# Performance work log

Hardware: AMD Instinct MI355X
Metric: run time of the kernel (lower is better)

The kernel has to match this reference:

```python
import jax, jax.numpy as jnp
import numpy as np

B, T, FIN, D = 8, 512, 256, 128


def setup_inputs() -> dict:
    key = jax.random.key(0)
    ks = jax.random.split(key, 12)
    s = lambda fan_in: 1.0 / np.sqrt(fan_in)
    return {
        "x": jax.random.normal(ks[0], (B, T, FIN), jnp.float32),
        "S0": jnp.zeros((B, 1, D, D), jnp.float32),
        "Z0": jnp.zeros((B, 1, D), jnp.float32),
        "gamma": jnp.ones((FIN,), jnp.float32),
        "beta": jnp.zeros((FIN,), jnp.float32),
        "Wk": jax.random.normal(ks[1], (FIN, D), jnp.float32) * s(FIN),
        "Wq": jax.random.normal(ks[2], (FIN, D), jnp.float32) * s(FIN),
        "Wv": jax.random.normal(ks[3], (FIN, D), jnp.float32) * s(FIN),
        "W1": jax.random.normal(ks[4], (D, D), jnp.float32) * s(D),
        "b1": jnp.zeros((D,), jnp.float32),
        "W2": jax.random.normal(ks[5], (D, D), jnp.float32) * s(D),
        "b2": jnp.zeros((D,), jnp.float32),
        "Ws": jax.random.normal(ks[6], (FIN, D), jnp.float32) * s(FIN),
        "bs": jnp.zeros((D,), jnp.float32),
    }


def reference(x, S0, Z0, gamma, beta, Wk, Wq, Wv, W1, b1, W2, b2, Ws, bs):
    CLAMP = 1e20
    # LayerNorm over feature dim
    mu = jnp.mean(x, axis=-1, keepdims=True)
    var = jnp.var(x, axis=-1, keepdims=True)
    xn = (x - mu) / jnp.sqrt(var + 1e-5) * gamma + beta
    # phi(x) = elu(x) + 1
    K = jax.nn.elu(xn @ Wk) + 1.0  # [B,T,D]
    Q = jax.nn.elu(xn @ Wq) + 1.0  # [B,T,D]
    V = xn @ Wv                     # [B,T,D]
    # outer-product state recurrence via cumsum (faithful to original)
    outer = jnp.einsum('bti,btj->btij', K, V)            # [B,T,D,D]
    S = jnp.clip(jnp.cumsum(outer, axis=1), -CLAMP, CLAMP) + S0  # [B,T,D,D]
    Z = jnp.clip(jnp.cumsum(K, axis=1), -CLAMP, CLAMP) + Z0      # [B,T,D]
    numerator = jnp.einsum('bti,btil->btl', Q, S)        # [B,T,D]
    denominator = jnp.einsum('bti,bti->bt', Q, Z)[..., None] + 1e-5
    out = numerator / denominator
    # FFN: relu(relu(out W1 + b1) W2 + b2)
    out = jax.nn.relu(jax.nn.relu(out @ W1 + b1) @ W2 + b2)
    # residual shortcut from normed input
    out = out + xn @ Ws + bs
    S_out = S.reshape(B, T, D * D)
    return out, S_out, Z
```

## Files before the change

kernel.cpp:

```cpp
#include <hip/hip_runtime.h>


constexpr int BB = 8, TT = 512, FIN_ = 256, DD = 128;
constexpr int NROW = BB * TT;
constexpr int CLEN = 64, NCH = 8;
constexpr float CLAMPV = 1e20f;

__global__ __launch_bounds__(256) void ln_kernel(
    const float* __restrict__ x, const float* __restrict__ gamma,
    const float* __restrict__ beta, float* __restrict__ xn)
{
  int row = blockIdx.x, tid = threadIdx.x;
  float v = x[row * FIN_ + tid];
  __shared__ float s1[256], s2[256];
  s1[tid] = v; s2[tid] = v * v;
  __syncthreads();
  for (int s = 128; s > 0; s >>= 1) {
    if (tid < s) { s1[tid] += s1[tid + s]; s2[tid] += s2[tid + s]; }
    __syncthreads();
  }
  float mu  = s1[0] * (1.0f / FIN_);
  float var = s2[0] * (1.0f / FIN_) - mu * mu;
  float rs  = rsqrtf(var + 1e-5f);
  xn[row * FIN_ + tid] = (v - mu) * rs * gamma[tid] + beta[tid];
}

__global__ __launch_bounds__(256) void gemm_qkvs(
    const float* __restrict__ xn,
    const float* __restrict__ Wk, const float* __restrict__ Wq,
    const float* __restrict__ Wv, const float* __restrict__ Ws,
    const float* __restrict__ bs,
    float* __restrict__ Kb, float* __restrict__ Qb,
    float* __restrict__ Vb, float* __restrict__ Rb)
{
  int ct = blockIdx.x, rt = blockIdx.y;
  int mat = ct >> 1, cb = (ct & 1) * 64;
  const float* W = (mat == 0) ? Wk : (mat == 1) ? Wq : (mat == 2) ? Wv : Ws;
  float* Ob      = (mat == 0) ? Kb : (mat == 1) ? Qb : (mat == 2) ? Vb : Rb;
  __shared__ float As[16][64];
  __shared__ float Bs[16][64];
  int tid = threadIdx.x;
  int tn = tid & 15, tm = tid >> 4;
  int lm = tid >> 2, lq = tid & 3;
  int lk = tid >> 4, ln4 = (tid & 15) * 4;
  float acc[4][4] = {};
  for (int k0 = 0; k0 < FIN_; k0 += 16) {
    float4 av = *(const float4*)&xn[(rt * 64 + lm) * FIN_ + k0 + lq * 4];
    As[lq * 4 + 0][lm] = av.x;
    As[lq * 4 + 1][lm] = av.y;
    As[lq * 4 + 2][lm] = av.z;
    As[lq * 4 + 3][lm] = av.w;
    *(float4*)&Bs[lk][ln4] = *(const float4*)&W[(k0 + lk) * DD + cb + ln4];
    __syncthreads();
#pragma unroll
    for (int k = 0; k < 16; k++) {
      float4 a = *(const float4*)&As[k][tm * 4];
      float4 b = *(const float4*)&Bs[k][tn * 4];
      float ar[4] = {a.x, a.y, a.z, a.w};
      float br[4] = {b.x, b.y, b.z, b.w};
#pragma unroll
      for (int i = 0; i < 4; i++)
#pragma unroll
        for (int j = 0; j < 4; j++) acc[i][j] += ar[i] * br[j];
    }
    __syncthreads();
  }
#pragma unroll
  for (int i = 0; i < 4; i++) {
    int row = rt * 64 + tm * 4 + i;
    int col = cb + tn * 4;
    float vals[4];
#pragma unroll
    for (int j = 0; j < 4; j++) {
      float v = acc[i][j];
      if (mat <= 1) v = (v > 0.f) ? v + 1.f : expf(v);
      else if (mat == 3) v += bs[col + j];
      vals[j] = v;
    }
    float4 o = make_float4(vals[0], vals[1], vals[2], vals[3]);
    *(float4*)&Ob[row * DD + col] = o;
  }
}

__global__ __launch_bounds__(256) void chunksum_kernel(
    const float* __restrict__ Kb, const float* __restrict__ Vb,
    float* __restrict__ chunkS, float* __restrict__ chunkz)
{
  int c = blockIdx.x, b = blockIdx.y, tid = threadIdx.x;
  __shared__ float Ks[CLEN][DD];
  const float* Kc = Kb + (b * TT + c * CLEN) * DD;
  const float* Vc = Vb + (b * TT + c * CLEN) * DD;
  for (int u = 0; u < 8; u++) {
    int idx = u * 256 + tid;
    int t = idx >> 5, c4 = (idx & 31) * 4;
    *(float4*)&Ks[t][c4] = *(const float4*)&Kc[t * DD + c4];
  }
  __syncthreads();
  int ti = tid >> 4, tj = tid & 15;
  int i0 = ti * 8, j0 = tj * 8;
  float acc[8][8] = {};
  for (int t = 0; t < CLEN; t++) {
    float kv[8], vv[8];
    *(float4*)&kv[0] = *(const float4*)&Ks[t][i0];
    *(float4*)&kv[4] = *(const float4*)&Ks[t][i0 + 4];
    *(float4*)&vv[0] = *(const float4*)&Vc[t * DD + j0];
    *(float4*)&vv[4] = *(const float4*)&Vc[t * DD + j0 + 4];
#pragma unroll
    for (int i = 0; i < 8; i++)
#pragma unroll
      for (int j = 0; j < 8; j++) acc[i][j] += kv[i] * vv[j];
  }
  float* oS = chunkS + (b * NCH + c) * DD * DD;
#pragma unroll
  for (int i = 0; i < 8; i++) {
    *(float4*)&oS[(i0 + i) * DD + j0]     = *(float4*)&acc[i][0];
    *(float4*)&oS[(i0 + i) * DD + j0 + 4] = *(float4*)&acc[i][4];
  }
  if (tid < DD) {
    float z = 0.f;
    for (int t = 0; t < CLEN; t++) z += Ks[t][tid];
    chunkz[(b * NCH + c) * DD + tid] = z;
  }
}

__global__ __launch_bounds__(256) void scan_s_kernel(
    const float* __restrict__ chunkS, const float* __restrict__ S0,
    float* __restrict__ prefS)
{
  int b = blockIdx.y;
  int idx = blockIdx.x * 256 + threadIdx.x;
  float s0v = S0[b * DD * DD + idx];
  float acc = 0.f;
  for (int c = 0; c < NCH; c++) {
    prefS[(b * NCH + c) * DD * DD + idx] = acc + s0v;
    acc += chunkS[(b * NCH + c) * DD * DD + idx];
  }
}

__global__ __launch_bounds__(128) void scan_z_kernel(
    const float* __restrict__ chunkz, const float* __restrict__ Z0,
    float* __restrict__ prefz)
{
  int b = blockIdx.x, i = threadIdx.x;
  float z0v = Z0[b * DD + i];
  float acc = 0.f;
  for (int c = 0; c < NCH; c++) {
    prefz[(b * NCH + c) * DD + i] = acc + z0v;
    acc += chunkz[(b * NCH + c) * DD + i];
  }
}

__global__ __launch_bounds__(256) void s_write_kernel(
    const float* __restrict__ Kb, const float* __restrict__ Vb,
    const float* __restrict__ prefS, float* __restrict__ Sout)
{
  int jt = blockIdx.x, c = blockIdx.y, b = blockIdx.z;
  __shared__ float Ks[CLEN][DD];
  __shared__ float Vs[CLEN][32];
  int tid = threadIdx.x;
  const float* Kc = Kb + (b * TT + c * CLEN) * DD;
  const float* Vc = Vb + (b * TT + c * CLEN) * DD + jt * 32;
  for (int u = 0; u < 8; u++) {
    int idx = u * 256 + tid;
    int t = idx >> 5, c4 = (idx & 31) * 4;
    *(float4*)&Ks[t][c4] = *(const float4*)&Kc[t * DD + c4];
  }
  for (int u = 0; u < 2; u++) {
    int idx = u * 256 + tid;
    int t = idx >> 3, c4 = (idx & 7) * 4;
    *(float4*)&Vs[t][c4] = *(const float4*)&Vc[t * DD + c4];
  }
  __syncthreads();
  int jq = tid & 7, irow = tid >> 3;
  int j = jt * 32 + jq * 4;
  float4 pref[4], acc[4];
#pragma unroll
  for (int p = 0; p < 4; p++) {
    int i = irow + 32 * p;
    pref[p] = *(const float4*)&prefS[(b * NCH + c) * DD * DD + i * DD + j];
    acc[p] = make_float4(0.f, 0.f, 0.f, 0.f);
  }
  float* So = Sout + (size_t)(b * TT + c * CLEN) * (DD * DD);
  for (int t = 0; t < CLEN; t++) {
    float4 v4 = *(const float4*)&Vs[t][jq * 4];
#pragma unroll
    for (int p = 0; p < 4; p++) {
      int i = irow + 32 * p;
      float kk = Ks[t][i];
      acc[p].x += kk * v4.x; acc[p].y += kk * v4.y;
      acc[p].z += kk * v4.z; acc[p].w += kk * v4.w;
      float4 o;
      o.x = fminf(fmaxf(pref[p].x + acc[p].x, -CLAMPV), CLAMPV);
      o.y = fminf(fmaxf(pref[p].y + acc[p].y, -CLAMPV), CLAMPV);
      o.z = fminf(fmaxf(pref[p].z + acc[p].z, -CLAMPV), CLAMPV);
      o.w = fminf(fmaxf(pref[p].w + acc[p].w, -CLAMPV), CLAMPV);
      *(float4*)&So[(size_t)t * (DD * DD) + i * DD + j] = o;
    }
  }
}

__global__ __launch_bounds__(256) void attn_a_kernel(
    const float* __restrict__ Kb, const float* __restrict__ Qb,
    const float* __restrict__ prefz, float* __restrict__ scores,
    float* __restrict__ Zout)
{
  int c = blockIdx.x, b = blockIdx.y, tid = threadIdx.x;
  __shared__ float KsT[DD][CLEN + 1];
  __shared__ float sc[CLEN][65];
  __shared__ float zeff[DD];
  const float* Kc = Kb + (b * TT + c * CLEN) * DD;
  const float* Qc = Qb + (b * TT + c * CLEN) * DD;
  for (int u = 0; u < 8; u++) {
    int idx = u * 256 + tid;
    int t = idx >> 5, c4 = (idx & 31) * 4;
    float4 v = *(const float4*)&Kc[t * DD + c4];
    KsT[c4 + 0][t] = v.x; KsT[c4 + 1][t] = v.y;
    KsT[c4 + 2][t] = v.z; KsT[c4 + 3][t] = v.w;
  }
  if (tid < DD) zeff[tid] = prefz[(b * NCH + c) * DD + tid];
  __syncthreads();
  int tn = tid & 15, tm = tid >> 4;
  float s[4][4] = {};
  for (int k4 = 0; k4 < 32; k4++) {
    float qv[4][4];
#pragma unroll
    for (int i = 0; i < 4; i++)
      *(float4*)&qv[i][0] = *(const float4*)&Qc[(tm * 4 + i) * DD + k4 * 4];
#pragma unroll
    for (int kk = 0; kk < 4; kk++) {
      int k = k4 * 4 + kk;
      float kv[4];
#pragma unroll
      for (int j = 0; j < 4; j++) kv[j] = KsT[k][tn * 4 + j];
#pragma unroll
      for (int i = 0; i < 4; i++)
#pragma unroll
        for (int j = 0; j < 4; j++) s[i][j] += qv[i][kk] * kv[j];
    }
  }
#pragma unroll
  for (int i = 0; i < 4; i++)
#pragma unroll
    for (int j = 0; j < 4; j++) {
      int t = tm * 4 + i, tau = tn * 4 + j;
      sc[t][tau] = (tau <= t) ? s[i][j] : 0.f;
    }
  __syncthreads();
  float* scg = scores + (b * NCH + c) * (CLEN * CLEN);
  for (int u = 0; u < 16; u++) {
    int idx = u * 256 + tid;
    scg[idx] = sc[idx >> 6][idx & 63];
  }
  if (tid < DD) {
    int i = tid;
    float a = zeff[i];
    for (int t = 0; t < CLEN; t++) {
      a += KsT[i][t];
      Zout[(size_t)(b * TT + c * CLEN + t) * DD + i] = fminf(fmaxf(a, -CLAMPV), CLAMPV);
    }
  }
}

__global__ __launch_bounds__(256) void attn_b_kernel(
    const float* __restrict__ Qb, const float* __restrict__ Vb,
    const float* __restrict__ prefS, const float* __restrict__ prefz,
    const float* __restrict__ scores, float* __restrict__ attn_o)
{
  int c = blockIdx.x, b = blockIdx.y, tid = threadIdx.x;
  __shared__ float Qs[CLEN][129];
  __shared__ float sc[CLEN][65];
  __shared__ float zeff[DD];
  __shared__ float den[CLEN];
  const float* Qc = Qb + (b * TT + c * CLEN) * DD;
  const float* Vc = Vb + (b * TT + c * CLEN) * DD;
  for (int u = 0; u < 8; u++) {
    int idx = u * 256 + tid;
    int t = idx >> 5, c4 = (idx & 31) * 4;
    float4 v = *(const float4*)&Qc[t * DD + c4];
    Qs[t][c4 + 0] = v.x; Qs[t][c4 + 1] = v.y;
    Qs[t][c4 + 2] = v.z; Qs[t][c4 + 3] = v.w;
  }
  const float* scg = scores + (b * NCH + c) * CLEN * CLEN;
  for (int u = 0; u < 16; u++) {
    int idx = u * 256 + tid;
    sc[idx >> 6][idx & 63] = scg[idx];
  }
  if (tid < DD) zeff[tid] = prefz[(b * NCH + c) * DD + tid];
  __syncthreads();
  if (tid < CLEN) {
    int t = tid;
    float d = 0.f;
    for (int tau = 0; tau < CLEN; tau++) d += sc[t][tau];
    float dz = 0.f;
    for (int k = 0; k < DD; k++) dz += Qs[t][k] * zeff[k];
    den[t] = d + dz + 1e-5f;
  }
  __syncthreads();
  int tl = tid & 31, tt = tid >> 5;
  int l0 = tl * 4, t0 = tt * 8;
  float num[8][4] = {};
  for (int tau = 0; tau < CLEN; tau++) {
    float4 v4 = *(const float4*)&Vc[tau * DD + l0];
    float ss[8];
#pragma unroll
    for (int ii = 0; ii < 8; ii++) ss[ii] = sc[t0 + ii][tau];
#pragma unroll
    for (int ii = 0; ii < 8; ii++) {
      num[ii][0] += ss[ii] * v4.x; num[ii][1] += ss[ii] * v4.y;
      num[ii][2] += ss[ii] * v4.z; num[ii][3] += ss[ii] * v4.w;
    }
  }
  const float* P = prefS + (b * NCH + c) * DD * DD;
  for (int i = 0; i < DD; i++) {
    float4 p4 = *(const float4*)&P[i * DD + l0];
    float qq[8];
#pragma unroll
    for (int ii = 0; ii < 8; ii++) qq[ii] = Qs[t0 + ii][i];
#pragma unroll
    for (int ii = 0; ii < 8; ii++) {
      num[ii][0] += qq[ii] * p4.x; num[ii][1] += qq[ii] * p4.y;
      num[ii][2] += qq[ii] * p4.z; num[ii][3] += qq[ii] * p4.w;
    }
  }
  float* og = attn_o + (size_t)(b * TT + c * CLEN) * DD;
#pragma unroll
  for (int ii = 0; ii < 8; ii++) {
    float dd = den[t0 + ii];
    float4 o = make_float4(num[ii][0] / dd, num[ii][1] / dd,
                           num[ii][2] / dd, num[ii][3] / dd);
    *(float4*)&og[(t0 + ii) * DD + l0] = o;
  }
}

__global__ __launch_bounds__(256) void ffn_kernel(
    const float* __restrict__ att, const float* __restrict__ res,
    const float* __restrict__ W1, const float* __restrict__ b1,
    const float* __restrict__ W2, const float* __restrict__ b2,
    float* __restrict__ outp)
{
  int rt = blockIdx.x, tid = threadIdx.x;
  __shared__ float As[32][129];
  __shared__ float H1[32][129];
  const float* ab = att + rt * 32 * DD;
  for (int u = 0; u < 4; u++) {
    int idx = u * 256 + tid;
    int r = idx >> 5, c4 = (idx & 31) * 4;
    float4 v = *(const float4*)&ab[r * DD + c4];
    As[r][c4 + 0] = v.x; As[r][c4 + 1] = v.y;
    As[r][c4 + 2] = v.z; As[r][c4 + 3] = v.w;
  }
  __syncthreads();
  int cn = tid & 31, rm = tid >> 5;
  int col = cn * 4, r0 = rm * 4;
  float acc[4][4] = {};
  for (int k = 0; k < DD; k++) {
    float4 w = *(const float4*)&W1[k * DD + col];
    float a[4];
#pragma unroll
    for (int i = 0; i < 4; i++) a[i] = As[r0 + i][k];
#pragma unroll
    for (int i = 0; i < 4; i++) {
      acc[i][0] += a[i] * w.x; acc[i][1] += a[i] * w.y;
      acc[i][2] += a[i] * w.z; acc[i][3] += a[i] * w.w;
    }
  }
  float4 bv = *(const float4*)&b1[col];
#pragma unroll
  for (int i = 0; i < 4; i++) {
    H1[r0 + i][col + 0] = fmaxf(acc[i][0] + bv.x, 0.f);
    H1[r0 + i][col + 1] = fmaxf(acc[i][1] + bv.y, 0.f);
    H1[r0 + i][col + 2] = fmaxf(acc[i][2] + bv.z, 0.f);
    H1[r0 + i][col + 3] = fmaxf(acc[i][3] + bv.w, 0.f);
  }
  __syncthreads();
  float acc2[4][4] = {};
  for (int k = 0; k < DD; k++) {
    float4 w = *(const float4*)&W2[k * DD + col];
    float a[4];
#pragma unroll
    for (int i = 0; i < 4; i++) a[i] = H1[r0 + i][k];
#pragma unroll
    for (int i = 0; i < 4; i++) {
      acc2[i][0] += a[i] * w.x; acc2[i][1] += a[i] * w.y;
      acc2[i][2] += a[i] * w.z; acc2[i][3] += a[i] * w.w;
    }
  }
  float4 b2v = *(const float4*)&b2[col];
#pragma unroll
  for (int i = 0; i < 4; i++) {
    int row = rt * 32 + r0 + i;
    float4 rv = *(const float4*)&res[row * DD + col];
    float4 o;
    o.x = fmaxf(acc2[i][0] + b2v.x, 0.f) + rv.x;
    o.y = fmaxf(acc2[i][1] + b2v.y, 0.f) + rv.y;
    o.z = fmaxf(acc2[i][2] + b2v.z, 0.f) + rv.z;
    o.w = fmaxf(acc2[i][3] + b2v.w, 0.f) + rv.w;
    *(float4*)&outp[row * DD + col] = o;
  }
}

extern "C" void kernel_launch(void* const* d_in, const int* in_sizes, int n_in,
                              void* d_out, int out_size, void* d_ws, size_t ws_size,
                              hipStream_t stream)
{
  const float* x     = (const float*)d_in[0];
  const float* S0    = (const float*)d_in[1];
  const float* Z0    = (const float*)d_in[2];
  const float* gamma = (const float*)d_in[3];
  const float* beta  = (const float*)d_in[4];
  const float* Wk    = (const float*)d_in[5];
  const float* Wq    = (const float*)d_in[6];
  const float* Wv    = (const float*)d_in[7];
  const float* W1    = (const float*)d_in[8];
  const float* b1    = (const float*)d_in[9];
  const float* W2    = (const float*)d_in[10];
  const float* b2    = (const float*)d_in[11];
  const float* Ws    = (const float*)d_in[12];
  const float* bs    = (const float*)d_in[13];

  float* out_main = (float*)d_out;
  float* Sout = out_main + NROW * DD;
  float* Zout = Sout + (size_t)NROW * DD * DD;

  float* ws_f   = (float*)d_ws;
  float* xn     = ws_f;
  float* Kb     = xn + 1048576;
  float* Qb     = Kb + 524288;
  float* Vb     = Qb + 524288;
  float* Rb     = Vb + 524288;
  float* chunkS = Rb + 524288;
  float* prefS  = chunkS + 1048576;
  float* chunkz = prefS + 1048576;
  float* prefz  = chunkz + 8192;
  float* scb    = prefz + 8192;
  float* attn_o = scb + 262144;

  ln_kernel<<<NROW, 256, 0, stream>>>(x, gamma, beta, xn);
  gemm_qkvs<<<dim3(8, 64), 256, 0, stream>>>(xn, Wk, Wq, Wv, Ws, bs, Kb, Qb, Vb, Rb);
  chunksum_kernel<<<dim3(NCH, BB), 256, 0, stream>>>(Kb, Vb, chunkS, chunkz);
  scan_s_kernel<<<dim3(64, BB), 256, 0, stream>>>(chunkS, S0, prefS);
  scan_z_kernel<<<BB, 128, 0, stream>>>(chunkz, Z0, prefz);
  s_write_kernel<<<dim3(4, NCH, BB), 256, 0, stream>>>(Kb, Vb, prefS, Sout);
  attn_a_kernel<<<dim3(NCH, BB), 256, 0, stream>>>(Kb, Qb, prefz, scb, Zout);
  attn_b_kernel<<<dim3(NCH, BB), 256, 0, stream>>>(Qb, Vb, prefS, prefz, scb, attn_o);
  ffn_kernel<<<NROW / 32, 256, 0, stream>>>(attn_o, Rb, W1, b1, W2, b2, out_main);
}
```

Baseline: 431.8 us.

## Widen grids for chunk and S-write kernels, fuse attention kernels, warp-shuffle LayerNorm

LayerNorm now uses one 64-lane wavefront per row with float4 loads and shuffle reductions instead of a shared-memory tree. The chunk-sum kernel is split across four column tiles and the S-write kernel across sixteen row tiles, giving more blocks for the 8x8 grids. The two attention kernels are merged so scores stay in shared memory instead of round-tripping through global memory. Shared memory per attention block grows, which may lower occupancy.

```diff
diff --git a/kernel.cpp b/kernel.cpp
--- a/kernel.cpp
+++ b/kernel.cpp
@@ -10,19 +10,28 @@
     const float* __restrict__ x, const float* __restrict__ gamma,
     const float* __restrict__ beta, float* __restrict__ xn)
 {
-  int row = blockIdx.x, tid = threadIdx.x;
-  float v = x[row * FIN_ + tid];
-  __shared__ float s1[256], s2[256];
-  s1[tid] = v; s2[tid] = v * v;
-  __syncthreads();
-  for (int s = 128; s > 0; s >>= 1) {
-    if (tid < s) { s1[tid] += s1[tid + s]; s2[tid] += s2[tid + s]; }
-    __syncthreads();
-  }
-  float mu  = s1[0] * (1.0f / FIN_);
-  float var = s2[0] * (1.0f / FIN_) - mu * mu;
+  int tid = threadIdx.x;
+  int row = blockIdx.x * 4 + (tid >> 6);
+  int lane = tid & 63;
+  float4 v = *(const float4*)&x[row * FIN_ + lane * 4];
+  float sum = v.x + v.y + v.z + v.w;
+  float sq  = v.x * v.x + v.y * v.y + v.z * v.z + v.w * v.w;
+#pragma unroll
+  for (int off = 1; off < 64; off <<= 1) {
+    sum += __shfl_xor(sum, off);
+    sq  += __shfl_xor(sq, off);
+  }
+  float mu  = sum * (1.0f / FIN_);
+  float var = sq * (1.0f / FIN_) - mu * mu;
   float rs  = rsqrtf(var + 1e-5f);
-  xn[row * FIN_ + tid] = (v - mu) * rs * gamma[tid] + beta[tid];
+  float4 g = *(const float4*)&gamma[lane * 4];
+  float4 b = *(const float4*)&beta[lane * 4];
+  float4 o;
+  o.x = (v.x - mu) * rs * g.x + b.x;
+  o.y = (v.y - mu) * rs * g.y + b.y;
+  o.z = (v.z - mu) * rs * g.z + b.z;
+  o.w = (v.w - mu) * rs * g.w + b.w;
+  *(float4*)&xn[row * FIN_ + lane * 4] = o;
 }
 
 __global__ __launch_bounds__(256) void gemm_qkvs(
@@ -86,37 +95,40 @@
     const float* __restrict__ Kb, const float* __restrict__ Vb,
     float* __restrict__ chunkS, float* __restrict__ chunkz)
 {
-  int c = blockIdx.x, b = blockIdx.y, tid = threadIdx.x;
+  int jt = blockIdx.x, c = blockIdx.y, b = blockIdx.z, tid = threadIdx.x;
   __shared__ float Ks[CLEN][DD];
+  __shared__ float Vs[CLEN][32];
   const float* Kc = Kb + (b * TT + c * CLEN) * DD;
-  const float* Vc = Vb + (b * TT + c * CLEN) * DD;
+  const float* Vc = Vb + (b * TT + c * CLEN) * DD + jt * 32;
   for (int u = 0; u < 8; u++) {
     int idx = u * 256 + tid;
     int t = idx >> 5, c4 = (idx & 31) * 4;
     *(float4*)&Ks[t][c4] = *(const float4*)&Kc[t * DD + c4];
   }
-  __syncthreads();
-  int ti = tid >> 4, tj = tid & 15;
-  int i0 = ti * 8, j0 = tj * 8;
-  float acc[8][8] = {};
+  for (int u = 0; u < 2; u++) {
+    int idx = u * 256 + tid;
+    int t = idx >> 3, c4 = (idx & 7) * 4;
+    *(float4*)&Vs[t][c4] = *(const float4*)&Vc[t * DD + c4];
+  }
+  __syncthreads();
+  int ti = tid >> 3, tj = tid & 7;
+  int i0 = ti * 4, jl = tj * 4;
+  float acc[4][4] = {};
   for (int t = 0; t < CLEN; t++) {
-    float kv[8], vv[8];
-    *(float4*)&kv[0] = *(const float4*)&Ks[t][i0];
-    *(float4*)&kv[4] = *(const float4*)&Ks[t][i0 + 4];
-    *(float4*)&vv[0] = *(const float4*)&Vc[t * DD + j0];
-    *(float4*)&vv[4] = *(const float4*)&Vc[t * DD + j0 + 4];
-#pragma unroll
-    for (int i = 0; i < 8; i++)
-#pragma unroll
-      for (int j = 0; j < 8; j++) acc[i][j] += kv[i] * vv[j];
-  }
-  float* oS = chunkS + (b * NCH + c) * DD * DD;
-#pragma unroll
-  for (int i = 0; i < 8; i++) {
-    *(float4*)&oS[(i0 + i) * DD + j0]     = *(float4*)&acc[i][0];
-    *(float4*)&oS[(i0 + i) * DD + j0 + 4] = *(float4*)&acc[i][4];
-  }
-  if (tid < DD) {
+    float4 kv = *(const float4*)&Ks[t][i0];
+    float4 vv = *(const float4*)&Vs[t][jl];
+    float kr[4] = {kv.x, kv.y, kv.z, kv.w};
+    float vr[4] = {vv.x, vv.y, vv.z, vv.w};
+#pragma unroll
+    for (int i = 0; i < 4; i++)
+#pragma unroll
+      for (int j = 0; j < 4; j++) acc[i][j] += kr[i] * vr[j];
+  }
+  float* oS = chunkS + (b * NCH + c) * DD * DD + jt * 32;
+#pragma unroll
+  for (int i = 0; i < 4; i++)
+    *(float4*)&oS[(i0 + i) * DD + jl] = *(float4*)&acc[i][0];
+  if (jt == 0 && tid < DD) {
     float z = 0.f;
     for (int t = 0; t < CLEN; t++) z += Ks[t][tid];
     chunkz[(b * NCH + c) * DD + tid] = z;
@@ -154,102 +166,97 @@
     const float* __restrict__ Kb, const float* __restrict__ Vb,
     const float* __restrict__ prefS, float* __restrict__ Sout)
 {
-  int jt = blockIdx.x, c = blockIdx.y, b = blockIdx.z;
-  __shared__ float Ks[CLEN][DD];
-  __shared__ float Vs[CLEN][32];
+  int it = blockIdx.x, c = blockIdx.y, b = blockIdx.z;
+  int i0 = it * 8;
+  __shared__ float Vs[CLEN][DD];
+  __shared__ float Ksm[CLEN][8];
   int tid = threadIdx.x;
   const float* Kc = Kb + (b * TT + c * CLEN) * DD;
-  const float* Vc = Vb + (b * TT + c * CLEN) * DD + jt * 32;
+  const float* Vc = Vb + (b * TT + c * CLEN) * DD;
   for (int u = 0; u < 8; u++) {
     int idx = u * 256 + tid;
     int t = idx >> 5, c4 = (idx & 31) * 4;
-    *(float4*)&Ks[t][c4] = *(const float4*)&Kc[t * DD + c4];
+    *(float4*)&Vs[t][c4] = *(const float4*)&Vc[t * DD + c4];
   }
   for (int u = 0; u < 2; u++) {
     int idx = u * 256 + tid;
-    int t = idx >> 3, c4 = (idx & 7) * 4;
-    *(float4*)&Vs[t][c4] = *(const float4*)&Vc[t * DD + c4];
-  }
-  __syncthreads();
-  int jq = tid & 7, irow = tid >> 3;
-  int j = jt * 32 + jq * 4;
-  float4 pref[4], acc[4];
-#pragma unroll
-  for (int p = 0; p < 4; p++) {
-    int i = irow + 32 * p;
-    pref[p] = *(const float4*)&prefS[(b * NCH + c) * DD * DD + i * DD + j];
-    acc[p] = make_float4(0.f, 0.f, 0.f, 0.f);
-  }
-  float* So = Sout + (size_t)(b * TT + c * CLEN) * (DD * DD);
+    int t = idx >> 3, r = idx & 7;
+    Ksm[t][r] = Kc[t * DD + i0 + r];
+  }
+  __syncthreads();
+  int irow = tid >> 5, jq = tid & 31;
+  int j = jq * 4;
+  float4 pref = *(const float4*)&prefS[(b * NCH + c) * DD * DD + (i0 + irow) * DD + j];
+  float4 acc = make_float4(0.f, 0.f, 0.f, 0.f);
+  float* So = Sout + (size_t)(b * TT + c * CLEN) * (DD * DD) + (i0 + irow) * DD + j;
   for (int t = 0; t < CLEN; t++) {
-    float4 v4 = *(const float4*)&Vs[t][jq * 4];
-#pragma unroll
-    for (int p = 0; p < 4; p++) {
-      int i = irow + 32 * p;
-      float kk = Ks[t][i];
-      acc[p].x += kk * v4.x; acc[p].y += kk * v4.y;
-      acc[p].z += kk * v4.z; acc[p].w += kk * v4.w;
-      float4 o;
-      o.x = fminf(fmaxf(pref[p].x + acc[p].x, -CLAMPV), CLAMPV);
-      o.y = fminf(fmaxf(pref[p].y + acc[p].y, -CLAMPV), CLAMPV);
-      o.z = fminf(fmaxf(pref[p].z + acc[p].z, -CLAMPV), CLAMPV);
-      o.w = fminf(fmaxf(pref[p].w + acc[p].w, -CLAMPV), CLAMPV);
-      *(float4*)&So[(size_t)t * (DD * DD) + i * DD + j] = o;
-    }
-  }
-}
-
-__global__ __launch_bounds__(256) void attn_a_kernel(
+    float4 v4 = *(const float4*)&Vs[t][j];
+    float kk = Ksm[t][irow];
+    acc.x += kk * v4.x; acc.y += kk * v4.y;
+    acc.z += kk * v4.z; acc.w += kk * v4.w;
+    float4 o;
+    o.x = fminf(fmaxf(pref.x + acc.x, -CLAMPV), CLAMPV);
+    o.y = fminf(fmaxf(pref.y + acc.y, -CLAMPV), CLAMPV);
+    o.z = fminf(fmaxf(pref.z + acc.z, -CLAMPV), CLAMPV);
+    o.w = fminf(fmaxf(pref.w + acc.w, -CLAMPV), CLAMPV);
+    *(float4*)&So[(size_t)t * (DD * DD)] = o;
+  }
+}
+
+__global__ __launch_bounds__(256) void attn_kernel(
     const float* __restrict__ Kb, const float* __restrict__ Qb,
-    const float* __restrict__ prefz, float* __restrict__ scores,
-    float* __restrict__ Zout)
+    const float* __restrict__ Vb, const float* __restrict__ prefS,
+    const float* __restrict__ prefz,
+    float* __restrict__ Zout, float* __restrict__ attn_o)
 {
   int c = blockIdx.x, b = blockIdx.y, tid = threadIdx.x;
   __shared__ float KsT[DD][CLEN + 1];
+  __shared__ float Qs[CLEN][DD + 1];
   __shared__ float sc[CLEN][65];
   __shared__ float zeff[DD];
+  __shared__ float den[CLEN];
   const float* Kc = Kb + (b * TT + c * CLEN) * DD;
   const float* Qc = Qb + (b * TT + c * CLEN) * DD;
+  const float* Vc = Vb + (b * TT + c * CLEN) * DD;
   for (int u = 0; u < 8; u++) {
     int idx = u * 256 + tid;
     int t = idx >> 5, c4 = (idx & 31) * 4;
     float4 v = *(const float4*)&Kc[t * DD + c4];
     KsT[c4 + 0][t] = v.x; KsT[c4 + 1][t] = v.y;
     KsT[c4 + 2][t] = v.z; KsT[c4 + 3][t] = v.w;
+    float4 q = *(const float4*)&Qc[t * DD + c4];
+    Qs[t][c4 + 0] = q.x; Qs[t][c4 + 1] = q.y;
+    Qs[t][c4 + 2] = q.z; Qs[t][c4 + 3] = q.w;
   }
   if (tid < DD) zeff[tid] = prefz[(b * NCH + c) * DD + tid];
   __syncthreads();
-  int tn = tid & 15, tm = tid >> 4;
-  float s[4][4] = {};
-  for (int k4 = 0; k4 < 32; k4++) {
-    float qv[4][4];
+  {
+    int tn = tid & 15, tm = tid >> 4;
+    float s[4][4] = {};
+    for (int k4 = 0; k4 < 32; k4++) {
+      float qv[4][4];
+#pragma unroll
+      for (int i = 0; i < 4; i++)
+        *(float4*)&qv[i][0] = *(const float4*)&Qc[(tm * 4 + i) * DD + k4 * 4];
+#pragma unroll
+      for (int kk = 0; kk < 4; kk++) {
+        int k = k4 * 4 + kk;
+        float kv[4];
+#pragma unroll
+        for (int j = 0; j < 4; j++) kv[j] = KsT[k][tn * 4 + j];
+#pragma unroll
+        for (int i = 0; i < 4; i++)
+#pragma unroll
+          for (int j = 0; j < 4; j++) s[i][j] += qv[i][kk] * kv[j];
+      }
+    }
 #pragma unroll
     for (int i = 0; i < 4; i++)
-      *(float4*)&qv[i][0] = *(const float4*)&Qc[(tm * 4 + i) * DD + k4 * 4];
-#pragma unroll
-    for (int kk = 0; kk < 4; kk++) {
-      int k = k4 * 4 + kk;
-      float kv[4];
-#pragma unroll
-      for (int j = 0; j < 4; j++) kv[j] = KsT[k][tn * 4 + j];
-#pragma unroll
-      for (int i = 0; i < 4; i++)
-#pragma unroll
-        for (int j = 0; j < 4; j++) s[i][j] += qv[i][kk] * kv[j];
-    }
-  }
-#pragma unroll
-  for (int i = 0; i < 4; i++)
-#pragma unroll
-    for (int j = 0; j < 4; j++) {
-      int t = tm * 4 + i, tau = tn * 4 + j;
-      sc[t][tau] = (tau <= t) ? s[i][j] : 0.f;
-    }
-  __syncthreads();
-  float* scg = scores + (b * NCH + c) * (CLEN * CLEN);
-  for (int u = 0; u < 16; u++) {
-    int idx = u * 256 + tid;
-    scg[idx] = sc[idx >> 6][idx & 63];
+#pragma unroll
+      for (int j = 0; j < 4; j++) {
+        int t = tm * 4 + i, tau = tn * 4 + j;
+        sc[t][tau] = (tau <= t) ? s[i][j] : 0.f;
+      }
   }
   if (tid < DD) {
     int i = tid;
@@ -259,33 +266,6 @@
       Zout[(size_t)(b * TT + c * CLEN + t) * DD + i] = fminf(fmaxf(a, -CLAMPV), CLAMPV);
     }
   }
-}
-
-__global__ __launch_bounds__(256) void attn_b_kernel(
-    const float* __restrict__ Qb, const float* __restrict__ Vb,
-    const float* __restrict__ prefS, const float* __restrict__ prefz,
-    const float* __restrict__ scores, float* __restrict__ attn_o)
-{
-  int c = blockIdx.x, b = blockIdx.y, tid = threadIdx.x;
-  __shared__ float Qs[CLEN][129];
-  __shared__ float sc[CLEN][65];
-  __shared__ float zeff[DD];
-  __shared__ float den[CLEN];
-  const float* Qc = Qb + (b * TT + c * CLEN) * DD;
-  const float* Vc = Vb + (b * TT + c * CLEN) * DD;
-  for (int u = 0; u < 8; u++) {
-    int idx = u * 256 + tid;
-    int t = idx >> 5, c4 = (idx & 31) * 4;
-    float4 v = *(const float4*)&Qc[t * DD + c4];
-    Qs[t][c4 + 0] = v.x; Qs[t][c4 + 1] = v.y;
-    Qs[t][c4 + 2] = v.z; Qs[t][c4 + 3] = v.w;
-  }
-  const float* scg = scores + (b * NCH + c) * CLEN * CLEN;
-  for (int u = 0; u < 16; u++) {
-    int idx = u * 256 + tid;
-    sc[idx >> 6][idx & 63] = scg[idx];
-  }
-  if (tid < DD) zeff[tid] = prefz[(b * NCH + c) * DD + tid];
   __syncthreads();
   if (tid < CLEN) {
     int t = tid;
@@ -432,16 +412,14 @@
   float* prefS  = chunkS + 1048576;
   float* chunkz = prefS + 1048576;
   float* prefz  = chunkz + 8192;
-  float* scb    = prefz + 8192;
-  float* attn_o = scb + 262144;
-
-  ln_kernel<<<NROW, 256, 0, stream>>>(x, gamma, beta, xn);
+  float* attn_o = prefz + 8192;
+
+  ln_kernel<<<NROW / 4, 256, 0, stream>>>(x, gamma, beta, xn);
   gemm_qkvs<<<dim3(8, 64), 256, 0, stream>>>(xn, Wk, Wq, Wv, Ws, bs, Kb, Qb, Vb, Rb);
-  chunksum_kernel<<<dim3(NCH, BB), 256, 0, stream>>>(Kb, Vb, chunkS, chunkz);
+  chunksum_kernel<<<dim3(4, NCH, BB), 256, 0, stream>>>(Kb, Vb, chunkS, chunkz);
   scan_s_kernel<<<dim3(64, BB), 256, 0, stream>>>(chunkS, S0, prefS);
   scan_z_kernel<<<BB, 128, 0, stream>>>(chunkz, Z0, prefz);
-  s_write_kernel<<<dim3(4, NCH, BB), 256, 0, stream>>>(Kb, Vb, prefS, Sout);
-  attn_a_kernel<<<dim3(NCH, BB), 256, 0, stream>>>(Kb, Qb, prefz, scb, Zout);
-  attn_b_kernel<<<dim3(NCH, BB), 256, 0, stream>>>(Qb, Vb, prefS, prefz, scb, attn_o);
+  s_write_kernel<<<dim3(16, NCH, BB), 256, 0, stream>>>(Kb, Vb, prefS, Sout);
+  attn_kernel<<<dim3(NCH, BB), 256, 0, stream>>>(Kb, Qb, Vb, prefS, prefz, Zout, attn_o);
   ffn_kernel<<<NROW / 32, 256, 0, stream>>>(attn_o, Rb, W1, b1, W2, b2, out_main);
 }
```

Result: faster. 417.6 us (-3.3%).
